# Kernel tuning notes

Measured on AMD Instinct MI355X. Metric: run time of the kernel, lower is better.

## Reference

```python
import jax, jax.numpy as jnp
import numpy as np

B, T, C, H = 4, 4096, 1024, 64

def setup_inputs() -> dict:
    key = jax.random.key(0)
    kx, kq, kk, kv = jax.random.split(key, 4)
    x = jax.random.normal(kx, (B, T, C), dtype=jnp.float32)
    Wq = jax.random.normal(kq, (C, H), dtype=jnp.float32) * (C ** -0.5)
    Wk = jax.random.normal(kk, (C, H), dtype=jnp.float32) * (C ** -0.5)
    Wv = jax.random.normal(kv, (C, H), dtype=jnp.float32) * (C ** -0.5)
    return {"x": x, "Wq": Wq, "Wk": Wk, "Wv": Wv}

def reference(x, Wq, Wk, Wv):
    # single-head causal attention, dropout p=0 (eval)
    q = jnp.einsum('btc,ch->bth', x, Wq)  # [B,T,H]
    k = jnp.einsum('btc,ch->bth', x, Wk)
    v = jnp.einsum('btc,ch->bth', x, Wv)
    scale = k.shape[-1] ** -0.5
    scores = jnp.einsum('bth,bsh->bts', q, k) * scale  # [B,T,T]
    causal = jnp.tril(jnp.ones((q.shape[1], q.shape[1]), dtype=bool))
    scores = jnp.where(causal, scores, -jnp.inf)
    weights = jax.nn.softmax(scores, axis=-1)
    out = jnp.einsum('bts,bsh->bth', weights, v)  # [B,T,H]
    return out
```

## Files before the change

kernel.cpp:

```cpp
#include <hip/hip_runtime.h>


typedef short  s16x8 __attribute__((ext_vector_type(8)));
typedef float  f32x4 __attribute__((ext_vector_type(4)));
typedef unsigned u32x2 __attribute__((ext_vector_type(2)));

constexpr int B = 4, T = 4096, C = 1024, H = 64;
constexpr int M = B * T;
constexpr float LOG2E = 1.44269504088896340736f;
constexpr float QSCALE = 0.125f * LOG2E;
constexpr float MBASE  = 4.0f * LOG2E;

__device__ __forceinline__ unsigned short f2bf(float f) {
    union { float f; unsigned u; } v; v.f = f;
    unsigned r = v.u + 0x7fffu + ((v.u >> 16) & 1u);
    return (unsigned short)(r >> 16);
}

__device__ __forceinline__ unsigned cvt_pk_bf16(float lo, float hi) {
    unsigned r;
    asm("v_cvt_pk_bf16_f32 %0, %1, %2" : "=v"(r) : "v"(lo), "v"(hi));
    return r;
}

__device__ __forceinline__ float vexp2(float x) {
    float r;
    asm("v_exp_f32 %0, %1" : "=v"(r) : "v"(x));
    return r;
}

__device__ __forceinline__ void gl_lds16(const void* g, void* l) {
    __builtin_amdgcn_global_load_lds(
        (const __attribute__((address_space(1))) unsigned*)g,
        (__attribute__((address_space(3))) unsigned*)l, 16, 0, 0);
}

__global__ void prep_w(const float* __restrict__ Wq, const float* __restrict__ Wk,
                       const float* __restrict__ Wv, unsigned short* __restrict__ Wt) {
    const int n = blockIdx.x;
    const float* W = (n < 64) ? Wq : (n < 128 ? Wk : Wv);
    const int col = n & 63;
    for (int k = threadIdx.x; k < C; k += blockDim.x)
        Wt[(size_t)n * C + k] = f2bf(W[(size_t)k * H + col]);
}

__global__ __launch_bounds__(512) void qkv_proj(
    const float* __restrict__ x, const unsigned short* __restrict__ Wt,
    unsigned short* __restrict__ Q, unsigned short* __restrict__ K,
    unsigned short* __restrict__ VT) {
    __shared__ __align__(16) unsigned short ldsA[2][32 * 64];
    __shared__ __align__(16) unsigned short ldsB[2][192 * 64];

    const int t = threadIdx.x, lane = t & 63, w = t >> 6;
    const int i = lane & 15, g = lane >> 4;
    const int rowbase = blockIdx.x * 32;
    const int rw = w & 1, nw = w >> 1;

    const int arow = t >> 3, aslot = t & 7;
    const float* aga = x + (size_t)(rowbase + arow) * C + ((aslot ^ (arow & 7)) * 8);
    const int awoff = arow * 64 + aslot * 8;
    const bool astage = (t < 256);

    const int brow8 = lane >> 3, bslot = lane & 7;
    const unsigned short* bga[3];
    int bn0[3];
#pragma unroll
    for (int j = 0; j < 3; ++j) {
        bn0[j] = w * 24 + j * 8;
        bga[j] = Wt + (size_t)(bn0[j] + brow8) * C + ((bslot ^ brow8) * 8);
    }

    f32x4 acc[3];
#pragma unroll
    for (int n = 0; n < 3; ++n) acc[n] = (f32x4){0.f, 0.f, 0.f, 0.f};

    {
#pragma unroll
        for (int j = 0; j < 3; ++j)
            gl_lds16(bga[j], &ldsB[0][bn0[j] * 64]);
        if (astage) {
            f32x4 a0 = *(const f32x4*)(aga);
            f32x4 a1 = *(const f32x4*)(aga + 4);
            union { unsigned u[4]; s16x8 v; } av;
            av.u[0] = cvt_pk_bf16(a0[0], a0[1]);
            av.u[1] = cvt_pk_bf16(a0[2], a0[3]);
            av.u[2] = cvt_pk_bf16(a1[0], a1[1]);
            av.u[3] = cvt_pk_bf16(a1[2], a1[3]);
            *(s16x8*)&ldsA[0][awoff] = av.v;
        }
    }
    __syncthreads();

    for (int it = 0; it < 16; ++it) {
        const int cur = it & 1, nxt = cur ^ 1;
        const int kc = (it + 1) * 64;
        f32x4 a0, a1;
        const bool more = (it < 15);
        if (more) {
            if (astage) {
                a0 = *(const f32x4*)(aga + kc);
                a1 = *(const f32x4*)(aga + kc + 4);
            }
#pragma unroll
            for (int j = 0; j < 3; ++j)
                gl_lds16(bga[j] + kc, &ldsB[nxt][bn0[j] * 64]);
        }
#pragma unroll
        for (int kst = 0; kst < 2; ++kst) {
            const int c = kst * 4 + g;
            s16x8 a = *(const s16x8*)&ldsA[cur][(rw * 16 + i) * 64 + ((c ^ (i & 7)) * 8)];
#pragma unroll
            for (int nt = 0; nt < 3; ++nt) {
                int n = nw * 48 + nt * 16 + i;
                s16x8 b = *(const s16x8*)&ldsB[cur][n * 64 + ((c ^ (i & 7)) * 8)];
                acc[nt] = __builtin_amdgcn_mfma_f32_16x16x32_bf16(a, b, acc[nt], 0, 0, 0);
            }
        }
        if (more && astage) {
            union { unsigned u[4]; s16x8 v; } av;
            av.u[0] = cvt_pk_bf16(a0[0], a0[1]);
            av.u[1] = cvt_pk_bf16(a0[2], a0[3]);
            av.u[2] = cvt_pk_bf16(a1[0], a1[1]);
            av.u[3] = cvt_pk_bf16(a1[2], a1[3]);
            *(s16x8*)&ldsA[nxt][awoff] = av.v;
        }
        __syncthreads();
    }

#pragma unroll
    for (int nt = 0; nt < 3; ++nt) {
        const int base = nw * 48 + nt * 16;
        const int n = base + i;
        if (base >= 128) {
            const int h = n - 128;
            const int bb = rowbase >> 12, tb = rowbase & 4095;
            u32x2 pk;
            pk[0] = cvt_pk_bf16(acc[nt][0], acc[nt][1]);
            pk[1] = cvt_pk_bf16(acc[nt][2], acc[nt][3]);
            *(u32x2*)(VT + (size_t)(bb * H + h) * T + tb + g * 8 + rw * 4) = pk;
        } else if (base >= 64) {
#pragma unroll
            for (int r = 0; r < 4; ++r)
                K[(size_t)(rowbase + rw * 16 + g * 4 + r) * H + (n - 64)] = f2bf(acc[nt][r]);
        } else {
#pragma unroll
            for (int r = 0; r < 4; ++r)
                Q[(size_t)(rowbase + rw * 16 + g * 4 + r) * H + n] = f2bf(acc[nt][r] * QSCALE);
        }
    }
}

template<int CUR>
__device__ __forceinline__ void attn_tile(
    int n, int nTiles, int sp, int q0w, int i, int g, int g4,
    int srow, int sl, int sx,
    const unsigned short* Kb, const unsigned short* Vb,
    unsigned short (&ks)[3][64 * 64], unsigned short (&vs)[3][64 * 64],
    const s16x8& bqa0, const s16x8& bqa1, const s16x8& bqb0, const s16x8& bqb1,
    const s16x8& ones, const f32x4& minit,
    f32x4 (&oa)[4], f32x4 (&ob)[4], f32x4& al, f32x4& bl) {
    constexpr int NXT = (CUR + 2) % 3;
    const int kv = (sp + n * 8) * 64;
    const bool issue = (n + 2 < nTiles);

    if (issue) {
        const int kvn = kv + 1024;
        gl_lds16(Kb + (size_t)(kvn + srow) * H + sx * 8, &ks[NXT][srow * 64 + sl * 8]);
        gl_lds16(Vb + (size_t)srow * T + kvn + sx * 8,   &vs[NXT][srow * 64 + sl * 8]);
    }

    if (kv <= q0w + 31) {
        s16x8 kb[8];
#pragma unroll
        for (int kst = 0; kst < 2; ++kst)
#pragma unroll
            for (int nt = 0; nt < 4; ++nt)
                kb[kst * 4 + nt] = *(const s16x8*)
                    &ks[CUR][(nt * 16 + i) * 64 + (((kst * 4 + g) ^ (i & 7)) * 8)];

        unsigned pa[8], pb2[8];

        {
            f32x4 s[4];
#pragma unroll
            for (int nt = 0; nt < 4; ++nt) {
                s[nt] = __builtin_amdgcn_mfma_f32_16x16x32_bf16(kb[nt], bqa0, minit, 0, 0, 0);
                s[nt] = __builtin_amdgcn_mfma_f32_16x16x32_bf16(kb[4 + nt], bqa1, s[nt], 0, 0, 0);
            }
            if (kv + 63 > q0w) {
                const int thr = q0w + i - kv;
#pragma unroll
                for (int nt = 0; nt < 4; ++nt)
#pragma unroll
                    for (int r = 0; r < 4; ++r)
                        if (nt * 16 + g4 + r > thr) s[nt][r] = -INFINITY;
            }
#pragma unroll
            for (int nt = 0; nt < 4; ++nt)
#pragma unroll
                for (int r = 0; r < 4; ++r)
                    s[nt][r] = vexp2(s[nt][r]);
#pragma unroll
            for (int nt = 0; nt < 4; ++nt) {
                pa[nt * 2]     = cvt_pk_bf16(s[nt][0], s[nt][1]);
                pa[nt * 2 + 1] = cvt_pk_bf16(s[nt][2], s[nt][3]);
            }
        }

        {
            f32x4 s[4];
#pragma unroll
            for (int nt = 0; nt < 4; ++nt) {
                s[nt] = __builtin_amdgcn_mfma_f32_16x16x32_bf16(kb[nt], bqb0, minit, 0, 0, 0);
                s[nt] = __builtin_amdgcn_mfma_f32_16x16x32_bf16(kb[4 + nt], bqb1, s[nt], 0, 0, 0);
            }
            if (kv + 63 > q0w + 16) {
                const int thr = q0w + 16 + i - kv;
#pragma unroll
                for (int nt = 0; nt < 4; ++nt)
#pragma unroll
                    for (int r = 0; r < 4; ++r)
                        if (nt * 16 + g4 + r > thr) s[nt][r] = -INFINITY;
            }
#pragma unroll
            for (int nt = 0; nt < 4; ++nt)
#pragma unroll
                for (int r = 0; r < 4; ++r)
                    s[nt][r] = vexp2(s[nt][r]);
#pragma unroll
            for (int nt = 0; nt < 4; ++nt) {
                pb2[nt * 2]     = cvt_pk_bf16(s[nt][0], s[nt][1]);
                pb2[nt * 2 + 1] = cvt_pk_bf16(s[nt][2], s[nt][3]);
            }
        }

        s16x8 vb[8];
#pragma unroll
        for (int kst = 0; kst < 2; ++kst)
#pragma unroll
            for (int nt = 0; nt < 4; ++nt)
                vb[kst * 4 + nt] = *(const s16x8*)
                    &vs[CUR][(nt * 16 + i) * 64 + (((kst * 4 + g) ^ (i & 7)) * 8)];

#pragma unroll
        for (int kst = 0; kst < 2; ++kst) {
            union { unsigned u[4]; s16x8 v; } fa, fb;
            fa.u[0] = pa[4 * kst];      fa.u[1] = pa[4 * kst + 1];
            fa.u[2] = pa[4 * kst + 2];  fa.u[3] = pa[4 * kst + 3];
            fb.u[0] = pb2[4 * kst];     fb.u[1] = pb2[4 * kst + 1];
            fb.u[2] = pb2[4 * kst + 2]; fb.u[3] = pb2[4 * kst + 3];
#pragma unroll
            for (int nt = 0; nt < 4; ++nt) {
                oa[nt] = __builtin_amdgcn_mfma_f32_16x16x32_bf16(vb[kst * 4 + nt], fa.v, oa[nt], 0, 0, 0);
                ob[nt] = __builtin_amdgcn_mfma_f32_16x16x32_bf16(vb[kst * 4 + nt], fb.v, ob[nt], 0, 0, 0);
            }
            al = __builtin_amdgcn_mfma_f32_16x16x32_bf16(ones, fa.v, al, 0, 0, 0);
            bl = __builtin_amdgcn_mfma_f32_16x16x32_bf16(ones, fb.v, bl, 0, 0, 0);
        }
    }

    if (issue) asm volatile("s_waitcnt vmcnt(2)\n\ts_barrier" ::: "memory");
    else       asm volatile("s_waitcnt vmcnt(0)\n\ts_barrier" ::: "memory");
}

__global__ __launch_bounds__(512) void attn(
    const unsigned short* __restrict__ Qg, const unsigned short* __restrict__ Kg,
    const unsigned short* __restrict__ VTg,
    unsigned short* __restrict__ Opb, float* __restrict__ lpart) {
    __shared__ __align__(16) unsigned short ks[3][64 * 64];
    __shared__ __align__(16) unsigned short vs[3][64 * 64];

    const int t = threadIdx.x, lane = t & 63, w = t >> 6;
    const int bid = blockIdx.x;
    const int b = bid & 3;
    const int sp = (bid >> 2) & 7;
    const int qt = 15 - (bid >> 5);
    const int q0 = qt * 256;
    const int q0w = q0 + w * 32;
    const int i = lane & 15, g = lane >> 4, g4 = g * 4;
    const int nkv = 4 * qt + 4;
    const int nTiles = (sp < nkv) ? ((nkv - sp + 7) >> 3) : 0;

    const unsigned short* Kb = Kg  + (size_t)b * T * H;
    const unsigned short* Vb = VTg + (size_t)b * H * T;

    const int srow = t >> 3, sl = t & 7, sx = sl ^ (srow & 7);

    const unsigned short* QrowA = Qg + (size_t)(b * T + q0w + i) * H;
    s16x8 bqa0 = *(const s16x8*)(QrowA + g * 8);
    s16x8 bqa1 = *(const s16x8*)(QrowA + 32 + g * 8);
    const unsigned short* QrowB = QrowA + 16 * H;
    s16x8 bqb0 = *(const s16x8*)(QrowB + g * 8);
    s16x8 bqb1 = *(const s16x8*)(QrowB + 32 + g * 8);

    const f32x4 minit = (f32x4){-MBASE, -MBASE, -MBASE, -MBASE};
    s16x8 ones;
#pragma unroll
    for (int j = 0; j < 8; ++j) ones[j] = (short)0x3F80;

    f32x4 oa[4], ob[4];
#pragma unroll
    for (int nt = 0; nt < 4; ++nt) {
        oa[nt] = (f32x4){0.f, 0.f, 0.f, 0.f};
        ob[nt] = (f32x4){0.f, 0.f, 0.f, 0.f};
    }
    f32x4 al = (f32x4){0.f, 0.f, 0.f, 0.f};
    f32x4 bl = (f32x4){0.f, 0.f, 0.f, 0.f};

    if (nTiles > 0) {
        const int kv0 = sp * 64;
        gl_lds16(Kb + (size_t)(kv0 + srow) * H + sx * 8, &ks[0][srow * 64 + sl * 8]);
        gl_lds16(Vb + (size_t)srow * T + kv0 + sx * 8,   &vs[0][srow * 64 + sl * 8]);
    }
    if (nTiles > 1) {
        const int kv1 = (sp + 8) * 64;
        gl_lds16(Kb + (size_t)(kv1 + srow) * H + sx * 8, &ks[1][srow * 64 + sl * 8]);
        gl_lds16(Vb + (size_t)srow * T + kv1 + sx * 8,   &vs[1][srow * 64 + sl * 8]);
        asm volatile("s_waitcnt vmcnt(2)\n\ts_barrier" ::: "memory");
    } else {
        asm volatile("s_waitcnt vmcnt(0)\n\ts_barrier" ::: "memory");
    }

    {
        int n = 0;
        while (n < nTiles) {
            attn_tile<0>(n, nTiles, sp, q0w, i, g, g4, srow, sl, sx, Kb, Vb,
                         ks, vs, bqa0, bqa1, bqb0, bqb1, ones, minit, oa, ob, al, bl);
            if (++n >= nTiles) break;
            attn_tile<1>(n, nTiles, sp, q0w, i, g, g4, srow, sl, sx, Kb, Vb,
                         ks, vs, bqa0, bqa1, bqb0, bqb1, ones, minit, oa, ob, al, bl);
            if (++n >= nTiles) break;
            attn_tile<2>(n, nTiles, sp, q0w, i, g, g4, srow, sl, sx, Kb, Vb,
                         ks, vs, bqa0, bqa1, bqb0, bqb1, ones, minit, oa, ob, al, bl);
            ++n;
        }
    }

    unsigned short* opA = Opb + ((size_t)bid * 256 + w * 32 + i) * 64;
    unsigned short* opB = opA + 16 * 64;
#pragma unroll
    for (int nt = 0; nt < 4; ++nt) {
        u32x2 pk;
        pk[0] = cvt_pk_bf16(oa[nt][0], oa[nt][1]);
        pk[1] = cvt_pk_bf16(oa[nt][2], oa[nt][3]);
        *(u32x2*)(opA + nt * 16 + g4) = pk;
        pk[0] = cvt_pk_bf16(ob[nt][0], ob[nt][1]);
        pk[1] = cvt_pk_bf16(ob[nt][2], ob[nt][3]);
        *(u32x2*)(opB + nt * 16 + g4) = pk;
    }
    if (g == 0) {
        lpart[(size_t)bid * 256 + w * 32 + i]      = al[0];
        lpart[(size_t)bid * 256 + w * 32 + 16 + i] = bl[0];
    }
}

__global__ __launch_bounds__(256) void merge8(
    const unsigned short* __restrict__ Opb, const float* __restrict__ lpart,
    float* __restrict__ out) {
    const int idx = blockIdx.x * 256 + threadIdx.x;
    const int row = idx >> 4, c4 = (idx & 15) * 4;
    const int b = row >> 12, q = row & 4095;
    const int qt = q >> 8, r = q & 255;
    const int qti = 15 - qt;

    float L = 0.f;
    f32x4 o = (f32x4){0.f, 0.f, 0.f, 0.f};
#pragma unroll
    for (int sp = 0; sp < 8; ++sp) {
        const int bidp = qti * 32 + sp * 4 + b;
        L += lpart[(size_t)bidp * 256 + r];
        union { unsigned long long d; unsigned short s[4]; } v;
        v.d = *(const unsigned long long*)&Opb[((size_t)bidp * 256 + r) * 64 + c4];
#pragma unroll
        for (int k = 0; k < 4; ++k) {
            union { unsigned u; float f; } cv;
            cv.u = (unsigned)v.s[k] << 16;
            o[k] += cv.f;
        }
    }
    const float inv = 1.0f / L;
    f32x4 res = (f32x4){o[0] * inv, o[1] * inv, o[2] * inv, o[3] * inv};
    *(f32x4*)&out[(size_t)row * 64 + c4] = res;
}

extern "C" void kernel_launch(void* const* d_in, const int* in_sizes, int n_in,
                              void* d_out, int out_size, void* d_ws, size_t ws_size,
                              hipStream_t stream) {
    (void)in_sizes; (void)n_in; (void)out_size; (void)ws_size;
    const float* x  = (const float*)d_in[0];
    const float* Wq = (const float*)d_in[1];
    const float* Wk = (const float*)d_in[2];
    const float* Wv = (const float*)d_in[3];
    float* out = (float*)d_out;

    char* ws = (char*)d_ws;
    unsigned short* Q  = (unsigned short*)(ws);
    unsigned short* K  = (unsigned short*)(ws + (size_t)1 * M * H * 2);
    unsigned short* VT = (unsigned short*)(ws + (size_t)3 * M * H * 2);
    unsigned short* Wt = (unsigned short*)(ws + (size_t)4 * M * H * 2);
    unsigned short* Opb = (unsigned short*)(ws + (size_t)4 * M * H * 2 + 512 * 1024);
    float* lpart = (float*)(ws + (size_t)4 * M * H * 2 + 512 * 1024
                            + (size_t)512 * 256 * 64 * 2);

    prep_w<<<192, 256, 0, stream>>>(Wq, Wk, Wv, Wt);
    qkv_proj<<<M / 32, 512, 0, stream>>>(x, Wt, Q, K, VT);
    attn<<<512, 512, 0, stream>>>(Q, K, VT, Opb, lpart);
    merge8<<<1024, 256, 0, stream>>>(Opb, lpart, out);
}
```

Measured before the change: 48.90 us.

## Give each wave 64 interleaved query rows and halve the attention grid

Each wave now handles four 16-row query groups, 64 rows in all, taken from interleaved 64-row blocks that pair early and late positions so causal work balances across waves. Each K/V tile staged in LDS is therefore reused for twice as many queries, and the grid shrinks from 512 to 256 blocks. The merge kernel's indexing is updated to match the new partial-output layout. The cost is more accumulator registers per wave, which may lower occupancy, and fewer blocks to fill the GPU.

Result: slower. 69.61 us (+42.4%).

```diff
diff --git a/kernel.cpp b/kernel.cpp
--- a/kernel.cpp
+++ b/kernel.cpp
@@ -156,9 +156,8 @@
     int srow, int sl, int sx,
     const unsigned short* Kb, const unsigned short* Vb,
     unsigned short (&ks)[3][64 * 64], unsigned short (&vs)[3][64 * 64],
-    const s16x8& bqa0, const s16x8& bqa1, const s16x8& bqb0, const s16x8& bqb1,
-    const s16x8& ones, const f32x4& minit,
-    f32x4 (&oa)[4], f32x4 (&ob)[4], f32x4& al, f32x4& bl) {
+    const s16x8 (&bq)[4][2], const s16x8& ones, const f32x4& minit,
+    f32x4 (&acc)[4][4], f32x4 (&lac)[4]) {
     constexpr int NXT = (CUR + 2) % 3;
     const int kv = (sp + n * 8) * 64;
     const bool issue = (n + 2 < nTiles);
@@ -169,7 +168,7 @@
         gl_lds16(Vb + (size_t)srow * T + kvn + sx * 8,   &vs[NXT][srow * 64 + sl * 8]);
     }
 
-    if (kv <= q0w + 31) {
+    if (kv <= q0w + 63) {
         s16x8 kb[8];
 #pragma unroll
         for (int kst = 0; kst < 2; ++kst)
@@ -178,59 +177,36 @@
                 kb[kst * 4 + nt] = *(const s16x8*)
                     &ks[CUR][(nt * 16 + i) * 64 + (((kst * 4 + g) ^ (i & 7)) * 8)];
 
-        unsigned pa[8], pb2[8];
-
-        {
-            f32x4 s[4];
-#pragma unroll
-            for (int nt = 0; nt < 4; ++nt) {
-                s[nt] = __builtin_amdgcn_mfma_f32_16x16x32_bf16(kb[nt], bqa0, minit, 0, 0, 0);
-                s[nt] = __builtin_amdgcn_mfma_f32_16x16x32_bf16(kb[4 + nt], bqa1, s[nt], 0, 0, 0);
-            }
-            if (kv + 63 > q0w) {
-                const int thr = q0w + i - kv;
+        unsigned pk[4][8];
+
+#pragma unroll
+        for (int grp = 0; grp < 4; ++grp) {
+            const int qg0 = q0w + grp * 16;
+            if (kv <= qg0 + 15) {
+                f32x4 s[4];
+#pragma unroll
+                for (int nt = 0; nt < 4; ++nt) {
+                    s[nt] = __builtin_amdgcn_mfma_f32_16x16x32_bf16(kb[nt], bq[grp][0], minit, 0, 0, 0);
+                    s[nt] = __builtin_amdgcn_mfma_f32_16x16x32_bf16(kb[4 + nt], bq[grp][1], s[nt], 0, 0, 0);
+                }
+                if (kv + 63 > qg0) {
+                    const int thr = qg0 + i - kv;
+#pragma unroll
+                    for (int nt = 0; nt < 4; ++nt)
+#pragma unroll
+                        for (int r = 0; r < 4; ++r)
+                            if (nt * 16 + g4 + r > thr) s[nt][r] = -INFINITY;
+                }
 #pragma unroll
                 for (int nt = 0; nt < 4; ++nt)
 #pragma unroll
                     for (int r = 0; r < 4; ++r)
-                        if (nt * 16 + g4 + r > thr) s[nt][r] = -INFINITY;
-            }
-#pragma unroll
-            for (int nt = 0; nt < 4; ++nt)
-#pragma unroll
-                for (int r = 0; r < 4; ++r)
-                    s[nt][r] = vexp2(s[nt][r]);
-#pragma unroll
-            for (int nt = 0; nt < 4; ++nt) {
-                pa[nt * 2]     = cvt_pk_bf16(s[nt][0], s[nt][1]);
-                pa[nt * 2 + 1] = cvt_pk_bf16(s[nt][2], s[nt][3]);
-            }
-        }
-
-        {
-            f32x4 s[4];
-#pragma unroll
-            for (int nt = 0; nt < 4; ++nt) {
-                s[nt] = __builtin_amdgcn_mfma_f32_16x16x32_bf16(kb[nt], bqb0, minit, 0, 0, 0);
-                s[nt] = __builtin_amdgcn_mfma_f32_16x16x32_bf16(kb[4 + nt], bqb1, s[nt], 0, 0, 0);
-            }
-            if (kv + 63 > q0w + 16) {
-                const int thr = q0w + 16 + i - kv;
-#pragma unroll
-                for (int nt = 0; nt < 4; ++nt)
-#pragma unroll
-                    for (int r = 0; r < 4; ++r)
-                        if (nt * 16 + g4 + r > thr) s[nt][r] = -INFINITY;
-            }
-#pragma unroll
-            for (int nt = 0; nt < 4; ++nt)
-#pragma unroll
-                for (int r = 0; r < 4; ++r)
-                    s[nt][r] = vexp2(s[nt][r]);
-#pragma unroll
-            for (int nt = 0; nt < 4; ++nt) {
-                pb2[nt * 2]     = cvt_pk_bf16(s[nt][0], s[nt][1]);
-                pb2[nt * 2 + 1] = cvt_pk_bf16(s[nt][2], s[nt][3]);
+                        s[nt][r] = vexp2(s[nt][r]);
+#pragma unroll
+                for (int nt = 0; nt < 4; ++nt) {
+                    pk[grp][nt * 2]     = cvt_pk_bf16(s[nt][0], s[nt][1]);
+                    pk[grp][nt * 2 + 1] = cvt_pk_bf16(s[nt][2], s[nt][3]);
+                }
             }
         }
 
@@ -243,19 +219,20 @@
                     &vs[CUR][(nt * 16 + i) * 64 + (((kst * 4 + g) ^ (i & 7)) * 8)];
 
 #pragma unroll
-        for (int kst = 0; kst < 2; ++kst) {
-            union { unsigned u[4]; s16x8 v; } fa, fb;
-            fa.u[0] = pa[4 * kst];      fa.u[1] = pa[4 * kst + 1];
-            fa.u[2] = pa[4 * kst + 2];  fa.u[3] = pa[4 * kst + 3];
-            fb.u[0] = pb2[4 * kst];     fb.u[1] = pb2[4 * kst + 1];
-            fb.u[2] = pb2[4 * kst + 2]; fb.u[3] = pb2[4 * kst + 3];
-#pragma unroll
-            for (int nt = 0; nt < 4; ++nt) {
-                oa[nt] = __builtin_amdgcn_mfma_f32_16x16x32_bf16(vb[kst * 4 + nt], fa.v, oa[nt], 0, 0, 0);
-                ob[nt] = __builtin_amdgcn_mfma_f32_16x16x32_bf16(vb[kst * 4 + nt], fb.v, ob[nt], 0, 0, 0);
+        for (int grp = 0; grp < 4; ++grp) {
+            if (kv <= q0w + grp * 16 + 15) {
+#pragma unroll
+                for (int kst = 0; kst < 2; ++kst) {
+                    union { unsigned u[4]; s16x8 v; } fa;
+                    fa.u[0] = pk[grp][4 * kst];     fa.u[1] = pk[grp][4 * kst + 1];
+                    fa.u[2] = pk[grp][4 * kst + 2]; fa.u[3] = pk[grp][4 * kst + 3];
+#pragma unroll
+                    for (int nt = 0; nt < 4; ++nt)
+                        acc[grp][nt] = __builtin_amdgcn_mfma_f32_16x16x32_bf16(
+                            vb[kst * 4 + nt], fa.v, acc[grp][nt], 0, 0, 0);
+                    lac[grp] = __builtin_amdgcn_mfma_f32_16x16x32_bf16(ones, fa.v, lac[grp], 0, 0, 0);
+                }
             }
-            al = __builtin_amdgcn_mfma_f32_16x16x32_bf16(ones, fa.v, al, 0, 0, 0);
-            bl = __builtin_amdgcn_mfma_f32_16x16x32_bf16(ones, fb.v, bl, 0, 0, 0);
         }
     }
 
@@ -273,41 +250,45 @@
     const int t = threadIdx.x, lane = t & 63, w = t >> 6;
     const int bid = blockIdx.x;
     const int b = bid & 3;
-    const int sp = (bid >> 2) & 7;
-    const int qt = 15 - (bid >> 5);
-    const int q0 = qt * 256;
-    const int q0w = q0 + w * 32;
+    const int rest = bid >> 2;
+    const int sp = rest & 7;
+    const int qti = rest >> 3;
+    const int qgi = (w < 4) ? w : (11 - w);
+    const int qg = qgi * 8 + qti;
+    const int q0w = qg * 64;
     const int i = lane & 15, g = lane >> 4, g4 = g * 4;
-    const int nkv = 4 * qt + 4;
-    const int nTiles = (sp < nkv) ? ((nkv - sp + 7) >> 3) : 0;
+    const int nTiles = ((56 + qti - sp) >> 3) + 1;
 
     const unsigned short* Kb = Kg  + (size_t)b * T * H;
     const unsigned short* Vb = VTg + (size_t)b * H * T;
 
     const int srow = t >> 3, sl = t & 7, sx = sl ^ (srow & 7);
 
-    const unsigned short* QrowA = Qg + (size_t)(b * T + q0w + i) * H;
-    s16x8 bqa0 = *(const s16x8*)(QrowA + g * 8);
-    s16x8 bqa1 = *(const s16x8*)(QrowA + 32 + g * 8);
-    const unsigned short* QrowB = QrowA + 16 * H;
-    s16x8 bqb0 = *(const s16x8*)(QrowB + g * 8);
-    s16x8 bqb1 = *(const s16x8*)(QrowB + 32 + g * 8);
+    s16x8 bq[4][2];
+    {
+        const unsigned short* Qbase = Qg + (size_t)(b * T + q0w + i) * H;
+#pragma unroll
+        for (int grp = 0; grp < 4; ++grp) {
+            bq[grp][0] = *(const s16x8*)(Qbase + (size_t)grp * 16 * H + g * 8);
+            bq[grp][1] = *(const s16x8*)(Qbase + (size_t)grp * 16 * H + 32 + g * 8);
+        }
+    }
 
     const f32x4 minit = (f32x4){-MBASE, -MBASE, -MBASE, -MBASE};
     s16x8 ones;
 #pragma unroll
     for (int j = 0; j < 8; ++j) ones[j] = (short)0x3F80;
 
-    f32x4 oa[4], ob[4];
-#pragma unroll
-    for (int nt = 0; nt < 4; ++nt) {
-        oa[nt] = (f32x4){0.f, 0.f, 0.f, 0.f};
-        ob[nt] = (f32x4){0.f, 0.f, 0.f, 0.f};
-    }
-    f32x4 al = (f32x4){0.f, 0.f, 0.f, 0.f};
-    f32x4 bl = (f32x4){0.f, 0.f, 0.f, 0.f};
-
-    if (nTiles > 0) {
+    f32x4 acc[4][4];
+    f32x4 lac[4];
+#pragma unroll
+    for (int grp = 0; grp < 4; ++grp) {
+        lac[grp] = (f32x4){0.f, 0.f, 0.f, 0.f};
+#pragma unroll
+        for (int nt = 0; nt < 4; ++nt) acc[grp][nt] = (f32x4){0.f, 0.f, 0.f, 0.f};
+    }
+
+    {
         const int kv0 = sp * 64;
         gl_lds16(Kb + (size_t)(kv0 + srow) * H + sx * 8, &ks[0][srow * 64 + sl * 8]);
         gl_lds16(Vb + (size_t)srow * T + kv0 + sx * 8,   &vs[0][srow * 64 + sl * 8]);
@@ -325,32 +306,30 @@
         int n = 0;
         while (n < nTiles) {
             attn_tile<0>(n, nTiles, sp, q0w, i, g, g4, srow, sl, sx, Kb, Vb,
-                         ks, vs, bqa0, bqa1, bqb0, bqb1, ones, minit, oa, ob, al, bl);
+                         ks, vs, bq, ones, minit, acc, lac);
             if (++n >= nTiles) break;
             attn_tile<1>(n, nTiles, sp, q0w, i, g, g4, srow, sl, sx, Kb, Vb,
-                         ks, vs, bqa0, bqa1, bqb0, bqb1, ones, minit, oa, ob, al, bl);
+                         ks, vs, bq, ones, minit, acc, lac);
             if (++n >= nTiles) break;
             attn_tile<2>(n, nTiles, sp, q0w, i, g, g4, srow, sl, sx, Kb, Vb,
-                         ks, vs, bqa0, bqa1, bqb0, bqb1, ones, minit, oa, ob, al, bl);
+                         ks, vs, bq, ones, minit, acc, lac);
             ++n;
         }
     }
 
-    unsigned short* opA = Opb + ((size_t)bid * 256 + w * 32 + i) * 64;
-    unsigned short* opB = opA + 16 * 64;
-#pragma unroll
-    for (int nt = 0; nt < 4; ++nt) {
-        u32x2 pk;
-        pk[0] = cvt_pk_bf16(oa[nt][0], oa[nt][1]);
-        pk[1] = cvt_pk_bf16(oa[nt][2], oa[nt][3]);
-        *(u32x2*)(opA + nt * 16 + g4) = pk;
-        pk[0] = cvt_pk_bf16(ob[nt][0], ob[nt][1]);
-        pk[1] = cvt_pk_bf16(ob[nt][2], ob[nt][3]);
-        *(u32x2*)(opB + nt * 16 + g4) = pk;
-    }
-    if (g == 0) {
-        lpart[(size_t)bid * 256 + w * 32 + i]      = al[0];
-        lpart[(size_t)bid * 256 + w * 32 + 16 + i] = bl[0];
+    unsigned short* opW = Opb + ((size_t)(bid * 8 + w) * 64) * 64;
+#pragma unroll
+    for (int grp = 0; grp < 4; ++grp) {
+        unsigned short* op = opW + (grp * 16 + i) * 64;
+#pragma unroll
+        for (int nt = 0; nt < 4; ++nt) {
+            u32x2 pk;
+            pk[0] = cvt_pk_bf16(acc[grp][nt][0], acc[grp][nt][1]);
+            pk[1] = cvt_pk_bf16(acc[grp][nt][2], acc[grp][nt][3]);
+            *(u32x2*)(op + nt * 16 + g4) = pk;
+        }
+        if (g == 0)
+            lpart[(size_t)(bid * 8 + w) * 64 + grp * 16 + i] = lac[grp][0];
     }
 }
 
@@ -360,17 +339,19 @@
     const int idx = blockIdx.x * 256 + threadIdx.x;
     const int row = idx >> 4, c4 = (idx & 15) * 4;
     const int b = row >> 12, q = row & 4095;
-    const int qt = q >> 8, r = q & 255;
-    const int qti = 15 - qt;
+    const int qg = q >> 6, r64 = q & 63;
+    const int qti = qg & 7, qgi = qg >> 3;
+    const int w = (qgi <= 3) ? qgi : (11 - qgi);
 
     float L = 0.f;
     f32x4 o = (f32x4){0.f, 0.f, 0.f, 0.f};
 #pragma unroll
     for (int sp = 0; sp < 8; ++sp) {
-        const int bidp = qti * 32 + sp * 4 + b;
-        L += lpart[(size_t)bidp * 256 + r];
+        const int bidp = (qti * 8 + sp) * 4 + b;
+        const size_t off = (size_t)(bidp * 8 + w) * 64 + r64;
+        L += lpart[off];
         union { unsigned long long d; unsigned short s[4]; } v;
-        v.d = *(const unsigned long long*)&Opb[((size_t)bidp * 256 + r) * 64 + c4];
+        v.d = *(const unsigned long long*)&Opb[off * 64 + c4];
 #pragma unroll
         for (int k = 0; k < 4; ++k) {
             union { unsigned u; float f; } cv;
@@ -400,10 +381,10 @@
     unsigned short* Wt = (unsigned short*)(ws + (size_t)4 * M * H * 2);
     unsigned short* Opb = (unsigned short*)(ws + (size_t)4 * M * H * 2 + 512 * 1024);
     float* lpart = (float*)(ws + (size_t)4 * M * H * 2 + 512 * 1024
-                            + (size_t)512 * 256 * 64 * 2);
+                            + (size_t)256 * 8 * 64 * 64 * 2);
 
     prep_w<<<192, 256, 0, stream>>>(Wq, Wk, Wv, Wt);
     qkv_proj<<<M / 32, 512, 0, stream>>>(x, Wt, Q, K, VT);
-    attn<<<512, 512, 0, stream>>>(Q, K, VT, Opb, lpart);
+    attn<<<256, 512, 0, stream>>>(Q, K, VT, Opb, lpart);
     merge8<<<1024, 256, 0, stream>>>(Opb, lpart, out);
 }
```
